# Kernel tuning notes

Hardware: AMD Instinct MI355X
Metric: run time of the kernel (lower is better)

## Reference

```python
import math
import jax, jax.numpy as jnp
import numpy as np
from jax import lax

MUL_IN, MUL_OUT = 8, 16
DIM_IN, DIM_OUT = 4 * MUL_IN, 4 * MUL_OUT  # 0e(1) + 1o(3) per multiplicity
DIAMETER = 3.0
STEPS = (1.0, 1.0, 1.0)
NUM_RB = 4
BATCH, GRID = 8, 32


def _lattice():
    r = DIAMETER / 2
    axes = [np.arange(-math.floor(r / s), math.floor(r / s) + 1.0) * s for s in STEPS]
    return jnp.asarray(np.stack(np.meshgrid(*axes, indexing='ij'), axis=-1), jnp.float32)  # [X,Y,Z,3]


def _sus(x):
    # smooth unit step: exp(-1/x) for x>0 else 0
    return jnp.where(x > 0.0, jnp.exp(-1.0 / jnp.where(x > 0.0, x, 1.0)), 0.0)


def _radial_emb(lattice):
    # soft_one_hot_linspace, basis='smooth_finite', cutoff=True
    dist = jnp.linalg.norm(lattice, axis=-1)
    values = jnp.linspace(0.0, DIAMETER / 2, NUM_RB + 2)
    step = values[1] - values[0]
    diff = (dist[..., None] - values[1:-1]) / step
    return 1.14136 * jnp.exp(2.0) * _sus(diff + 1.0) * _sus(1.0 - diff)  # [X,Y,Z,NUM_RB]


def _sph(lattice):
    # real spherical harmonics l=0,1; normalize=True, 'component' normalization
    norm = jnp.linalg.norm(lattice, axis=-1, keepdims=True)
    unit = lattice / jnp.where(norm == 0.0, 1.0, norm)
    sh0 = jnp.ones(lattice.shape[:-1] + (1,), lattice.dtype)
    sh1 = jnp.sqrt(jnp.float32(3.0)) * unit
    return sh0, sh1


def setup_inputs() -> dict:
    key = jax.random.key(0)
    ks = jax.random.split(key, 7)
    x = jax.random.normal(ks[0], (BATCH, GRID, GRID, GRID, DIM_IN), jnp.float32)
    w_lin0 = jax.random.normal(ks[1], (MUL_IN, MUL_OUT), jnp.float32)
    w_lin1 = jax.random.normal(ks[2], (MUL_IN, MUL_OUT), jnp.float32)
    pshape = (NUM_RB, MUL_IN, 1, MUL_OUT)
    w000 = jax.random.normal(ks[3], pshape, jnp.float32)
    w011 = jax.random.normal(ks[4], pshape, jnp.float32)
    w101 = jax.random.normal(ks[5], pshape, jnp.float32)
    w110 = jax.random.normal(ks[6], pshape, jnp.float32)
    return dict(x=x, w_lin0=w_lin0, w_lin1=w_lin1, w000=w000, w011=w011, w101=w101, w110=w110)


def _forward(x, w_lin0, w_lin1, w000, w011, w101, w110):
    lattice = _lattice()
    emb = _radial_emb(lattice)
    sh0, sh1 = _sph(lattice)
    n_lat = lattice.shape[0] * lattice.shape[1] * lattice.shape[2]

    # ---- self-connection: FunctionalLinear(irreps_in -> irreps_out), per-l blocks ----
    lin_norm = 1.0 / math.sqrt(MUL_IN)
    x0 = x[..., :MUL_IN]                                             # [B,X,Y,Z,8]
    x1 = x[..., MUL_IN:].reshape(x.shape[:-1] + (MUL_IN, 3))         # [B,X,Y,Z,8,3]
    sc0 = jnp.einsum('...u,uw->...w', x0, w_lin0) * lin_norm
    sc1 = (jnp.einsum('...ui,uw->...wi', x1, w_lin1) * lin_norm).reshape(x.shape[:-1] + (3 * MUL_OUT,))
    sc = jnp.concatenate([sc0, sc1], axis=-1)                        # [B,X,Y,Z,DIM_OUT]

    # ---- radial weights per lattice point: einsum('xyzk,k...->xyz...') / n_lat ----
    def rad(w):
        return jnp.einsum('xyzk,kuvw->xyzuw', emb, w) / n_lat        # sh mul v == 1 squeezed
    r000, r011, r101, r110 = rad(w000), rad(w011), rad(w101), rad(w110)

    # ---- CG tensor-product 'right': build kernel [X,Y,Z, DIM_IN, DIM_OUT] ----
    inv_s3 = 1.0 / math.sqrt(3.0)  # w3j(0,1,1)=w3j(1,0,1)=w3j(1,1,0)=eye/sqrt(3); w3j(0,0,0)=1
    alpha = 1.0 / math.sqrt(2.0 * MUL_IN)  # 2 paths feed each output irrep, fan mul_in each

    eye3 = jnp.eye(3, dtype=x.dtype)
    # in 0e x sh 0e -> out 0e
    k00 = alpha * r000 * sh0[..., 0][..., None, None]                 # [X,Y,Z,8,16]
    # in 0e x sh 1o -> out 1o
    k01 = (alpha * inv_s3) * jnp.einsum('xyzuw,xyzm->xyzuwm', r011, sh1)
    k01 = k01.reshape(k01.shape[:3] + (MUL_IN, 3 * MUL_OUT))          # [X,Y,Z,8,48]
    # in 1o x sh 1o -> out 0e
    k10 = (alpha * inv_s3) * jnp.einsum('xyzuw,xyzi->xyzuiw', r110, sh1)
    k10 = k10.reshape(k10.shape[:3] + (3 * MUL_IN, MUL_OUT))          # [X,Y,Z,24,16]
    # in 1o x sh 0e -> out 1o
    k11 = (alpha * inv_s3) * jnp.einsum('xyzuw,im->xyzuiwm', r101 * sh0[..., 0][..., None, None], eye3)
    k11 = k11.reshape(k11.shape[:3] + (3 * MUL_IN, 3 * MUL_OUT))      # [X,Y,Z,24,48]

    k = jnp.concatenate([
        jnp.concatenate([k00, k01], axis=-1),
        jnp.concatenate([k10, k11], axis=-1),
    ], axis=-2)                                                       # [X,Y,Z,DIM_IN,DIM_OUT]

    conv = lax.conv_general_dilated(
        lhs=x, rhs=k, window_strides=(1, 1, 1), padding='SAME',
        dimension_numbers=('NXYZC', 'XYZIO', 'NXYZC'))
    return sc + conv


def reference(x, w_lin0, w_lin1, w000, w011, w101, w110):
    return _forward(x, w_lin0, w_lin1, w000, w011, w101, w110)
```

## Files before the change

kernel.cpp:

```cpp
#include <hip/hip_runtime.h>


typedef __attribute__((ext_vector_type(8))) short bf16x8;
typedef __attribute__((ext_vector_type(4))) float f32x4;
typedef unsigned int u32;

__device__ __forceinline__ float sus_f(float v) { return v > 0.f ? __expf(-1.f / v) : 0.f; }

__device__ __forceinline__ unsigned short f2bf(float f) {
    union { float f; unsigned u; } c; c.f = f;
    unsigned u = c.u;
    u += 0x7FFFu + ((u >> 16) & 1u);
    return (unsigned short)(u >> 16);
}

__global__ __launch_bounds__(256) void prep_k(
    const float* __restrict__ w_lin0, const float* __restrict__ w_lin1,
    const float* __restrict__ w000,  const float* __restrict__ w011,
    const float* __restrict__ w101,  const float* __restrict__ w110,
    unsigned short* __restrict__ kw)
{
    const int taps[19] = {1,3,4,5,7,9,10,11,12,13,14,15,16,17,19,21,22,23,25};
    const int ta = blockIdx.x;
    const int t = taps[ta];
    const int a = t / 9, b = (t / 3) % 3, c = t % 3;

    const float fx = (float)(a - 1), fy = (float)(b - 1), fz = (float)(c - 1);
    const float dist = sqrtf(fx * fx + fy * fy + fz * fz);
    float emb[4];
    #pragma unroll
    for (int r = 0; r < 4; ++r) {
        const float v = 0.3f * (float)(r + 1);
        const float d = (dist - v) * (1.0f / 0.3f);
        emb[r] = 8.4335731f * sus_f(d + 1.f) * sus_f(1.f - d);
    }
    const float s = (dist > 0.f) ? (1.7320508f / dist) : 0.f;
    const float shv[3] = { fx * s, fy * s, fz * s };
    const float S000 = 0.25f / 27.f;
    const float S1   = 0.25f * 0.57735027f / 27.f;
    const float LNRM = 0.35355339f;

    const int tid = threadIdx.x;
    const int ci = tid >> 3;
    #pragma unroll
    for (int j = 0; j < 8; ++j) {
        const int o = (tid & 7) * 8 + j;
        float val;
        if (ci < 8) {
            const int u = ci;
            if (o < 16) {
                const float* p = w000 + u * 16 + o;
                val = S000 * (emb[0]*p[0] + emb[1]*p[128] + emb[2]*p[256] + emb[3]*p[384]);
                if (t == 13) val += LNRM * w_lin0[u * 16 + o];
            } else {
                const int oo = o - 16, w = oo / 3, m = oo % 3;
                const float* p = w011 + u * 16 + w;
                val = S1 * shv[m] * (emb[0]*p[0] + emb[1]*p[128] + emb[2]*p[256] + emb[3]*p[384]);
            }
        } else {
            const int iu = ci - 8, u = iu / 3, ic = iu % 3;
            if (o < 16) {
                const float* p = w110 + u * 16 + o;
                val = S1 * shv[ic] * (emb[0]*p[0] + emb[1]*p[128] + emb[2]*p[256] + emb[3]*p[384]);
            } else {
                const int oo = o - 16, w = oo / 3, m = oo % 3;
                if (ic == m) {
                    const float* p = w101 + u * 16 + w;
                    val = S1 * (emb[0]*p[0] + emb[1]*p[128] + emb[2]*p[256] + emb[3]*p[384]);
                    if (t == 13) val += LNRM * w_lin1[u * 16 + w];
                } else {
                    val = 0.f;
                }
            }
        }
        const int g = ci >> 3, slot = ci & 7, nt = o >> 4, cc = o & 15;
        const int lane = (g << 4) | cc;
        kw[((size_t)(ta * 4 + nt) * 64 + lane) * 8 + slot] = f2bf(val);
    }
}

__global__ __launch_bounds__(256, 2) void conv_fused(
    const float* __restrict__ x,
    const unsigned short* __restrict__ kw,
    float* __restrict__ out)
{
    __shared__ unsigned short lx[3 * 10 * 34 * 32];

    const int tid = threadIdx.x;
    const int bid = blockIdx.x;
    const int xcd = bid & 7, idx = bid >> 3;
    const int gid = xcd * 128 + idx;
    const int n = gid >> 7, X = (gid >> 2) & 31, Yg = gid & 3;
    const int Y0 = Yg * 8;
    const int wid = tid >> 6, l = tid & 63, lr = l & 15, lg = l >> 4;

    const bf16x8* kwf = reinterpret_cast<const bf16x8*>(kw);

    bf16x8 bring[4][4];
    #pragma unroll
    for (int p = 0; p < 3; ++p)
        #pragma unroll
        for (int nt = 0; nt < 4; ++nt)
            bring[p][nt] = kwf[(size_t)(p * 4 + nt) * 64 + l];

    if (tid < 60) {
        const int row = tid >> 1, zp = (tid & 1) * 33;
        f32x4* dp = reinterpret_cast<f32x4*>(
            reinterpret_cast<char*>(lx) + row * 2176 + zp * 64);
        #pragma unroll
        for (int q = 0; q < 4; ++q) dp[q] = (f32x4)0.f;
    }

    for (int it = tid; it < 960; it += 256) {
        const int dx = it / 320, rem = it - dx * 320;
        const int y6 = rem >> 5, z = rem & 31;
        const int gx = X + dx - 1, gy = Y0 + y6 - 1;
        char* row = reinterpret_cast<char*>(lx) + (dx * 10 + y6) * 2176 + (z + 1) * 64;
        if ((unsigned)gx < 32u && (unsigned)gy < 32u) {
            const float4* sp = reinterpret_cast<const float4*>(
                x + ((size_t)(((n * 32 + gx) * 32 + gy) * 32 + z) << 5));
            const int swz = ((z + 1) >> 1) & 3;
            #pragma unroll
            for (int g = 0; g < 4; ++g) {
                const float4 lo = sp[2 * g], hi = sp[2 * g + 1];
                bf16x8 w;
                w[0] = (short)f2bf(lo.x); w[1] = (short)f2bf(lo.y);
                w[2] = (short)f2bf(lo.z); w[3] = (short)f2bf(lo.w);
                w[4] = (short)f2bf(hi.x); w[5] = (short)f2bf(hi.y);
                w[6] = (short)f2bf(hi.z); w[7] = (short)f2bf(hi.w);
                *reinterpret_cast<bf16x8*>(row + ((g ^ swz) << 4)) = w;
            }
        } else {
            bf16x8 zz = (bf16x8)(short)0;
            #pragma unroll
            for (int g = 0; g < 4; ++g)
                *reinterpret_cast<bf16x8*>(row + (g << 4)) = zz;
        }
    }
    __syncthreads();

    constexpr int TA[19] = {1,3,4,5,7,9,10,11,12,13,14,15,16,17,19,21,22,23,25};
    const char* lxc = reinterpret_cast<const char*>(lx);
    const int yloc = wid * 2;

    f32x4 acc[4][4];
    #pragma unroll
    for (int r = 0; r < 4; ++r)
        #pragma unroll
        for (int nt = 0; nt < 4; ++nt) acc[r][nt] = (f32x4)0.f;

    #pragma unroll
    for (int ta = 0; ta < 19; ++ta) {
        const int t = TA[ta];
        const int a = t / 9, b = (t / 3) % 3, c = t % 3;

        if (ta + 3 < 19) {
            #pragma unroll
            for (int nt = 0; nt < 4; ++nt)
                bring[(ta + 3) & 3][nt] = kwf[(size_t)((ta + 3) * 4 + nt) * 64 + l];
        }

        bf16x8 af[4];
        #pragma unroll
        for (int r = 0; r < 4; ++r) {
            const int y10 = yloc + (r >> 1) + b;
            const int zp = 16 * (r & 1) + lr + c;
            const int byte = ((a * 10 + y10) * 34 + zp) * 64 + ((lg ^ ((zp >> 1) & 3)) << 4);
            af[r] = *reinterpret_cast<const bf16x8*>(lxc + byte);
        }

        #pragma unroll
        for (int r = 0; r < 4; ++r)
            #pragma unroll
            for (int nt = 0; nt < 4; ++nt)
                acc[r][nt] = __builtin_amdgcn_mfma_f32_16x16x32_bf16(
                    af[r], bring[ta & 3][nt], acc[r][nt], 0, 0, 0);
    }

    float* ob = out + ((size_t)(((n * 32 + X) * 32 + Y0 + yloc) * 32) << 6);
    #pragma unroll
    for (int r = 0; r < 4; ++r) {
        float* oy = ob + (size_t)(r >> 1) * 2048;
        #pragma unroll
        for (int nt = 0; nt < 4; ++nt)
            #pragma unroll
            for (int reg = 0; reg < 4; ++reg) {
                const int z = 16 * (r & 1) + 4 * lg + reg;
                oy[z * 64 + nt * 16 + lr] = acc[r][nt][reg];
            }
    }
}

extern "C" void kernel_launch(void* const* d_in, const int* in_sizes, int n_in,
                              void* d_out, int out_size, void* d_ws, size_t ws_size,
                              hipStream_t stream) {
    const float* x    = (const float*)d_in[0];
    const float* wl0  = (const float*)d_in[1];
    const float* wl1  = (const float*)d_in[2];
    const float* w000 = (const float*)d_in[3];
    const float* w011 = (const float*)d_in[4];
    const float* w101 = (const float*)d_in[5];
    const float* w110 = (const float*)d_in[6];
    float* out = (float*)d_out;
    unsigned short* kw = (unsigned short*)d_ws;

    prep_k<<<dim3(19), dim3(256), 0, stream>>>(wl0, wl1, w000, w011, w101, w110, kw);
    conv_fused<<<dim3(1024), dim3(256), 0, stream>>>(x, kw, out);
}
```

Baseline: 43.97 us.

## Halve conv tile to 4 Y rows per block, double grid, raise occupancy

Each block now covers 4 Y rows instead of 8, so the grid doubles to 2048 blocks and each wave handles one Y row with 2 z-halves. The LDS halo tile shrinks from 10 to 6 Y rows, and launch bounds ask for 4 blocks per CU, aiming for more latency hiding and better load balance. The fp32-to-bf16 conversion also switches to the HIP intrinsic. In exchange, the halo overhead per output rises from 10/8 to 6/4 rows, so more input is reloaded, and the MFMA count per shared B-fragment load is lower.

```diff
diff --git a/kernel.cpp b/kernel.cpp
--- a/kernel.cpp
+++ b/kernel.cpp
@@ -1,4 +1,5 @@
 #include <hip/hip_runtime.h>
+#include <hip/hip_bf16.h>
 
 
 typedef __attribute__((ext_vector_type(8))) short bf16x8;
@@ -12,6 +13,11 @@
     unsigned u = c.u;
     u += 0x7FFFu + ((u >> 16) & 1u);
     return (unsigned short)(u >> 16);
+}
+
+__device__ __forceinline__ short f2bf_fast(float f) {
+    __hip_bfloat16 h = __float2bfloat16(f);
+    return *reinterpret_cast<short*>(&h);
 }
 
 __global__ __launch_bounds__(256) void prep_k(
@@ -79,19 +85,18 @@
     }
 }
 
-__global__ __launch_bounds__(256, 2) void conv_fused(
+__global__ __launch_bounds__(256, 4) void conv_fused(
     const float* __restrict__ x,
     const unsigned short* __restrict__ kw,
     float* __restrict__ out)
 {
-    __shared__ unsigned short lx[3 * 10 * 34 * 32];
+    __shared__ unsigned short lx[3 * 6 * 34 * 32];
 
     const int tid = threadIdx.x;
     const int bid = blockIdx.x;
     const int xcd = bid & 7, idx = bid >> 3;
-    const int gid = xcd * 128 + idx;
-    const int n = gid >> 7, X = (gid >> 2) & 31, Yg = gid & 3;
-    const int Y0 = Yg * 8;
+    const int n = xcd, X = idx >> 3, Yg = idx & 7;
+    const int Y0 = Yg * 4;
     const int wid = tid >> 6, l = tid & 63, lr = l & 15, lg = l >> 4;
 
     const bf16x8* kwf = reinterpret_cast<const bf16x8*>(kw);
@@ -103,7 +108,7 @@
         for (int nt = 0; nt < 4; ++nt)
             bring[p][nt] = kwf[(size_t)(p * 4 + nt) * 64 + l];
 
-    if (tid < 60) {
+    if (tid < 36) {
         const int row = tid >> 1, zp = (tid & 1) * 33;
         f32x4* dp = reinterpret_cast<f32x4*>(
             reinterpret_cast<char*>(lx) + row * 2176 + zp * 64);
@@ -111,11 +116,11 @@
         for (int q = 0; q < 4; ++q) dp[q] = (f32x4)0.f;
     }
 
-    for (int it = tid; it < 960; it += 256) {
-        const int dx = it / 320, rem = it - dx * 320;
+    for (int it = tid; it < 576; it += 256) {
+        const int dx = it / 192, rem = it - dx * 192;
         const int y6 = rem >> 5, z = rem & 31;
         const int gx = X + dx - 1, gy = Y0 + y6 - 1;
-        char* row = reinterpret_cast<char*>(lx) + (dx * 10 + y6) * 2176 + (z + 1) * 64;
+        char* row = reinterpret_cast<char*>(lx) + (dx * 6 + y6) * 2176 + (z + 1) * 64;
         if ((unsigned)gx < 32u && (unsigned)gy < 32u) {
             const float4* sp = reinterpret_cast<const float4*>(
                 x + ((size_t)(((n * 32 + gx) * 32 + gy) * 32 + z) << 5));
@@ -124,10 +129,10 @@
             for (int g = 0; g < 4; ++g) {
                 const float4 lo = sp[2 * g], hi = sp[2 * g + 1];
                 bf16x8 w;
-                w[0] = (short)f2bf(lo.x); w[1] = (short)f2bf(lo.y);
-                w[2] = (short)f2bf(lo.z); w[3] = (short)f2bf(lo.w);
-                w[4] = (short)f2bf(hi.x); w[5] = (short)f2bf(hi.y);
-                w[6] = (short)f2bf(hi.z); w[7] = (short)f2bf(hi.w);
+                w[0] = f2bf_fast(lo.x); w[1] = f2bf_fast(lo.y);
+                w[2] = f2bf_fast(lo.z); w[3] = f2bf_fast(lo.w);
+                w[4] = f2bf_fast(hi.x); w[5] = f2bf_fast(hi.y);
+                w[6] = f2bf_fast(hi.z); w[7] = f2bf_fast(hi.w);
                 *reinterpret_cast<bf16x8*>(row + ((g ^ swz) << 4)) = w;
             }
         } else {
@@ -141,11 +146,10 @@
 
     constexpr int TA[19] = {1,3,4,5,7,9,10,11,12,13,14,15,16,17,19,21,22,23,25};
     const char* lxc = reinterpret_cast<const char*>(lx);
-    const int yloc = wid * 2;
-
-    f32x4 acc[4][4];
-    #pragma unroll
-    for (int r = 0; r < 4; ++r)
+
+    f32x4 acc[2][4];
+    #pragma unroll
+    for (int r = 0; r < 2; ++r)
         #pragma unroll
         for (int nt = 0; nt < 4; ++nt) acc[r][nt] = (f32x4)0.f;
 
@@ -160,35 +164,33 @@
                 bring[(ta + 3) & 3][nt] = kwf[(size_t)((ta + 3) * 4 + nt) * 64 + l];
         }
 
-        bf16x8 af[4];
-        #pragma unroll
-        for (int r = 0; r < 4; ++r) {
-            const int y10 = yloc + (r >> 1) + b;
-            const int zp = 16 * (r & 1) + lr + c;
-            const int byte = ((a * 10 + y10) * 34 + zp) * 64 + ((lg ^ ((zp >> 1) & 3)) << 4);
+        bf16x8 af[2];
+        #pragma unroll
+        for (int r = 0; r < 2; ++r) {
+            const int y6 = wid + b;
+            const int zp = 16 * r + lr + c;
+            const int byte = ((a * 6 + y6) * 34 + zp) * 64 + ((lg ^ ((zp >> 1) & 3)) << 4);
             af[r] = *reinterpret_cast<const bf16x8*>(lxc + byte);
         }
 
         #pragma unroll
-        for (int r = 0; r < 4; ++r)
+        for (int r = 0; r < 2; ++r)
             #pragma unroll
             for (int nt = 0; nt < 4; ++nt)
                 acc[r][nt] = __builtin_amdgcn_mfma_f32_16x16x32_bf16(
                     af[r], bring[ta & 3][nt], acc[r][nt], 0, 0, 0);
     }
 
-    float* ob = out + ((size_t)(((n * 32 + X) * 32 + Y0 + yloc) * 32) << 6);
-    #pragma unroll
-    for (int r = 0; r < 4; ++r) {
-        float* oy = ob + (size_t)(r >> 1) * 2048;
+    float* ob = out + ((size_t)(((n * 32 + X) * 32 + Y0 + wid) * 32) << 6);
+    #pragma unroll
+    for (int r = 0; r < 2; ++r)
         #pragma unroll
         for (int nt = 0; nt < 4; ++nt)
             #pragma unroll
             for (int reg = 0; reg < 4; ++reg) {
-                const int z = 16 * (r & 1) + 4 * lg + reg;
-                oy[z * 64 + nt * 16 + lr] = acc[r][nt][reg];
-            }
-    }
+                const int z = 16 * r + 4 * lg + reg;
+                ob[z * 64 + nt * 16 + lr] = acc[r][nt][reg];
+            }
 }
 
 extern "C" void kernel_launch(void* const* d_in, const int* in_sizes, int n_in,
@@ -205,5 +207,5 @@
     unsigned short* kw = (unsigned short*)d_ws;
 
     prep_k<<<dim3(19), dim3(256), 0, stream>>>(wl0, wl1, w000, w011, w101, w110, kw);
-    conv_fused<<<dim3(1024), dim3(256), 0, stream>>>(x, kw, out);
-}
+    conv_fused<<<dim3(2048), dim3(256), 0, stream>>>(x, kw, out);
+}
```

After: 53.55 us. +21.8%, slower.

## Walk two X planes per block with a rotating three-plane LDS buffer

Applied to the files above, without the earlier changes.

Each block now computes two consecutive X output planes. It keeps three staged input planes in LDS as a ring and loads only one new plane for the second output. This cuts redundant global loads and bf16 conversion of halo planes from three per output plane to two, and halves the grid to 512 blocks. It also switches to the library bf16 conversion. The trade-offs are an extra barrier mid-computation, less parallelism across the grid, and serialized staging between the two planes.

```diff
diff --git a/kernel.cpp b/kernel.cpp
--- a/kernel.cpp
+++ b/kernel.cpp
@@ -1,9 +1,11 @@
 #include <hip/hip_runtime.h>
+#include <hip/hip_bf16.h>
 
 
 typedef __attribute__((ext_vector_type(8))) short bf16x8;
 typedef __attribute__((ext_vector_type(4))) float f32x4;
-typedef unsigned int u32;
+
+__device__ constexpr int TAt[19] = {1,3,4,5,7,9,10,11,12,13,14,15,16,17,19,21,22,23,25};
 
 __device__ __forceinline__ float sus_f(float v) { return v > 0.f ? __expf(-1.f / v) : 0.f; }
 
@@ -12,6 +14,10 @@
     unsigned u = c.u;
     u += 0x7FFFu + ((u >> 16) & 1u);
     return (unsigned short)(u >> 16);
+}
+__device__ __forceinline__ short f2bf_fast(float f) {
+    __hip_bfloat16 h = __float2bfloat16(f);
+    return *reinterpret_cast<short*>(&h);
 }
 
 __global__ __launch_bounds__(256) void prep_k(
@@ -20,9 +26,8 @@
     const float* __restrict__ w101,  const float* __restrict__ w110,
     unsigned short* __restrict__ kw)
 {
-    const int taps[19] = {1,3,4,5,7,9,10,11,12,13,14,15,16,17,19,21,22,23,25};
     const int ta = blockIdx.x;
-    const int t = taps[ta];
+    const int t = TAt[ta];
     const int a = t / 9, b = (t / 3) % 3, c = t % 3;
 
     const float fx = (float)(a - 1), fy = (float)(b - 1), fz = (float)(c - 1);
@@ -79,7 +84,41 @@
     }
 }
 
-__global__ __launch_bounds__(256, 2) void conv_fused(
+template<int LO, int HI>
+__device__ __forceinline__ void tap_range(
+    const char* lxc, const bf16x8* kwf, int l, int lr, int lg, int yloc,
+    int s0, int s1, int s2, bf16x8 (&bring)[4][4], f32x4 (&acc)[4][4])
+{
+    #pragma unroll
+    for (int ta = LO; ta < HI; ++ta) {
+        const int t = TAt[ta];
+        const int a = t / 9, b = (t / 3) % 3, c = t % 3;
+
+        if (ta + 3 < 19) {
+            #pragma unroll
+            for (int nt = 0; nt < 4; ++nt)
+                bring[(ta + 3) & 3][nt] = kwf[(size_t)((ta + 3) * 4 + nt) * 64 + l];
+        }
+
+        const int sbase = (a == 0 ? s0 : (a == 1 ? s1 : s2)) * 21760;
+        bf16x8 af[4];
+        #pragma unroll
+        for (int r = 0; r < 4; ++r) {
+            const int y10 = yloc + (r >> 1) + b;
+            const int zp = 16 * (r & 1) + lr + c;
+            af[r] = *reinterpret_cast<const bf16x8*>(
+                lxc + sbase + (y10 * 34 + zp) * 64 + ((lg ^ ((zp >> 1) & 3)) << 4));
+        }
+        #pragma unroll
+        for (int r = 0; r < 4; ++r)
+            #pragma unroll
+            for (int nt = 0; nt < 4; ++nt)
+                acc[r][nt] = __builtin_amdgcn_mfma_f32_16x16x32_bf16(
+                    af[r], bring[ta & 3][nt], acc[r][nt], 0, 0, 0);
+    }
+}
+
+__global__ __launch_bounds__(256, 2) void conv_walk(
     const float* __restrict__ x,
     const unsigned short* __restrict__ kw,
     float* __restrict__ out)
@@ -88,107 +127,109 @@
 
     const int tid = threadIdx.x;
     const int bid = blockIdx.x;
-    const int xcd = bid & 7, idx = bid >> 3;
-    const int gid = xcd * 128 + idx;
-    const int n = gid >> 7, X = (gid >> 2) & 31, Yg = gid & 3;
+    const int n = bid & 7;
+    const int idx = bid >> 3;
+    const int Xc = idx >> 2, Yg = idx & 3;
+    const int X0 = Xc * 2;
     const int Y0 = Yg * 8;
     const int wid = tid >> 6, l = tid & 63, lr = l & 15, lg = l >> 4;
+    const int yloc = wid * 2;
 
     const bf16x8* kwf = reinterpret_cast<const bf16x8*>(kw);
+    char* lxc = reinterpret_cast<char*>(lx);
+
+    if (tid < 60) {
+        const int s = tid / 20, rem = tid % 20;
+        const int rr = rem >> 1, zp = (rem & 1) * 33;
+        f32x4* dp = reinterpret_cast<f32x4*>(lxc + s * 21760 + rr * 2176 + zp * 64);
+        #pragma unroll
+        for (int q = 0; q < 4; ++q) dp[q] = (f32x4)0.f;
+    }
+
+    auto stage_plane = [&](int p, int s) {
+        for (int it = tid; it < 320; it += 256) {
+            const int y6 = it >> 5, z = it & 31;
+            const int gy = Y0 + y6 - 1;
+            char* row = lxc + s * 21760 + y6 * 2176 + (z + 1) * 64;
+            if ((unsigned)p < 32u && (unsigned)gy < 32u) {
+                const float4* sp = reinterpret_cast<const float4*>(
+                    x + ((size_t)(((n * 32 + p) * 32 + gy) * 32 + z) << 5));
+                const int swz = ((z + 1) >> 1) & 3;
+                #pragma unroll
+                for (int g = 0; g < 4; ++g) {
+                    const float4 lo = sp[2 * g], hi = sp[2 * g + 1];
+                    bf16x8 w;
+                    w[0] = f2bf_fast(lo.x); w[1] = f2bf_fast(lo.y);
+                    w[2] = f2bf_fast(lo.z); w[3] = f2bf_fast(lo.w);
+                    w[4] = f2bf_fast(hi.x); w[5] = f2bf_fast(hi.y);
+                    w[6] = f2bf_fast(hi.z); w[7] = f2bf_fast(hi.w);
+                    *reinterpret_cast<bf16x8*>(row + ((g ^ swz) << 4)) = w;
+                }
+            } else {
+                bf16x8 zz = (bf16x8)(short)0;
+                #pragma unroll
+                for (int g = 0; g < 4; ++g)
+                    *reinterpret_cast<bf16x8*>(row + (g << 4)) = zz;
+            }
+        }
+    };
 
     bf16x8 bring[4][4];
-    #pragma unroll
-    for (int p = 0; p < 3; ++p)
-        #pragma unroll
-        for (int nt = 0; nt < 4; ++nt)
-            bring[p][nt] = kwf[(size_t)(p * 4 + nt) * 64 + l];
-
-    if (tid < 60) {
-        const int row = tid >> 1, zp = (tid & 1) * 33;
-        f32x4* dp = reinterpret_cast<f32x4*>(
-            reinterpret_cast<char*>(lx) + row * 2176 + zp * 64);
-        #pragma unroll
-        for (int q = 0; q < 4; ++q) dp[q] = (f32x4)0.f;
-    }
-
-    for (int it = tid; it < 960; it += 256) {
-        const int dx = it / 320, rem = it - dx * 320;
-        const int y6 = rem >> 5, z = rem & 31;
-        const int gx = X + dx - 1, gy = Y0 + y6 - 1;
-        char* row = reinterpret_cast<char*>(lx) + (dx * 10 + y6) * 2176 + (z + 1) * 64;
-        if ((unsigned)gx < 32u && (unsigned)gy < 32u) {
-            const float4* sp = reinterpret_cast<const float4*>(
-                x + ((size_t)(((n * 32 + gx) * 32 + gy) * 32 + z) << 5));
-            const int swz = ((z + 1) >> 1) & 3;
-            #pragma unroll
-            for (int g = 0; g < 4; ++g) {
-                const float4 lo = sp[2 * g], hi = sp[2 * g + 1];
-                bf16x8 w;
-                w[0] = (short)f2bf(lo.x); w[1] = (short)f2bf(lo.y);
-                w[2] = (short)f2bf(lo.z); w[3] = (short)f2bf(lo.w);
-                w[4] = (short)f2bf(hi.x); w[5] = (short)f2bf(hi.y);
-                w[6] = (short)f2bf(hi.z); w[7] = (short)f2bf(hi.w);
-                *reinterpret_cast<bf16x8*>(row + ((g ^ swz) << 4)) = w;
-            }
-        } else {
-            bf16x8 zz = (bf16x8)(short)0;
-            #pragma unroll
-            for (int g = 0; g < 4; ++g)
-                *reinterpret_cast<bf16x8*>(row + (g << 4)) = zz;
-        }
-    }
+    auto ring_preload = [&]() {
+        #pragma unroll
+        for (int p = 0; p < 3; ++p)
+            #pragma unroll
+            for (int nt = 0; nt < 4; ++nt)
+                bring[p][nt] = kwf[(size_t)(p * 4 + nt) * 64 + l];
+    };
+
+    auto epilogue = [&](int X, f32x4 (&acc)[4][4]) {
+        float* ob = out + ((size_t)(((n * 32 + X) * 32 + Y0 + yloc) * 32) << 6);
+        #pragma unroll
+        for (int r = 0; r < 4; ++r) {
+            float* oy = ob + (size_t)(r >> 1) * 2048;
+            #pragma unroll
+            for (int nt = 0; nt < 4; ++nt)
+                #pragma unroll
+                for (int reg = 0; reg < 4; ++reg) {
+                    const int z = 16 * (r & 1) + 4 * lg + reg;
+                    oy[z * 64 + nt * 16 + lr] = acc[r][nt][reg];
+                }
+        }
+    };
+
+    const int sm = (X0 + 2) % 3;
+    const int s0 = X0 % 3;
+    const int s1 = (X0 + 1) % 3;
+
+    ring_preload();
+    stage_plane(X0 - 1, sm);
+    stage_plane(X0,     s0);
+    stage_plane(X0 + 1, s1);
     __syncthreads();
 
-    constexpr int TA[19] = {1,3,4,5,7,9,10,11,12,13,14,15,16,17,19,21,22,23,25};
-    const char* lxc = reinterpret_cast<const char*>(lx);
-    const int yloc = wid * 2;
-
     f32x4 acc[4][4];
     #pragma unroll
     for (int r = 0; r < 4; ++r)
         #pragma unroll
         for (int nt = 0; nt < 4; ++nt) acc[r][nt] = (f32x4)0.f;
 
-    #pragma unroll
-    for (int ta = 0; ta < 19; ++ta) {
-        const int t = TA[ta];
-        const int a = t / 9, b = (t / 3) % 3, c = t % 3;
-
-        if (ta + 3 < 19) {
-            #pragma unroll
-            for (int nt = 0; nt < 4; ++nt)
-                bring[(ta + 3) & 3][nt] = kwf[(size_t)((ta + 3) * 4 + nt) * 64 + l];
-        }
-
-        bf16x8 af[4];
-        #pragma unroll
-        for (int r = 0; r < 4; ++r) {
-            const int y10 = yloc + (r >> 1) + b;
-            const int zp = 16 * (r & 1) + lr + c;
-            const int byte = ((a * 10 + y10) * 34 + zp) * 64 + ((lg ^ ((zp >> 1) & 3)) << 4);
-            af[r] = *reinterpret_cast<const bf16x8*>(lxc + byte);
-        }
-
-        #pragma unroll
-        for (int r = 0; r < 4; ++r)
-            #pragma unroll
-            for (int nt = 0; nt < 4; ++nt)
-                acc[r][nt] = __builtin_amdgcn_mfma_f32_16x16x32_bf16(
-                    af[r], bring[ta & 3][nt], acc[r][nt], 0, 0, 0);
-    }
-
-    float* ob = out + ((size_t)(((n * 32 + X) * 32 + Y0 + yloc) * 32) << 6);
-    #pragma unroll
-    for (int r = 0; r < 4; ++r) {
-        float* oy = ob + (size_t)(r >> 1) * 2048;
-        #pragma unroll
-        for (int nt = 0; nt < 4; ++nt)
-            #pragma unroll
-            for (int reg = 0; reg < 4; ++reg) {
-                const int z = 16 * (r & 1) + 4 * lg + reg;
-                oy[z * 64 + nt * 16 + lr] = acc[r][nt][reg];
-            }
-    }
+    tap_range<0, 5>(lxc, kwf, l, lr, lg, yloc, sm, s0, s1, bring, acc);
+    __syncthreads();
+    tap_range<5, 19>(lxc, kwf, l, lr, lg, yloc, sm, s0, s1, bring, acc);
+    epilogue(X0, acc);
+
+    stage_plane(X0 + 2, sm);
+    ring_preload();
+    __syncthreads();
+
+    #pragma unroll
+    for (int r = 0; r < 4; ++r)
+        #pragma unroll
+        for (int nt = 0; nt < 4; ++nt) acc[r][nt] = (f32x4)0.f;
+
+    tap_range<0, 19>(lxc, kwf, l, lr, lg, yloc, s0, s1, sm, bring, acc);
+    epilogue(X0 + 1, acc);
 }
 
 extern "C" void kernel_launch(void* const* d_in, const int* in_sizes, int n_in,
@@ -205,5 +246,5 @@
     unsigned short* kw = (unsigned short*)d_ws;
 
     prep_k<<<dim3(19), dim3(256), 0, stream>>>(wl0, wl1, w000, w011, w101, w110, kw);
-    conv_fused<<<dim3(1024), dim3(256), 0, stream>>>(x, kw, out);
-}
+    conv_walk<<<dim3(512), dim3(256), 0, stream>>>(x, kw, out);
+}
```

After: 62.58 us. 1.42x slower.
